# Kernel optimization log

Measured on AMD Instinct MI355X. Metric: run time of the kernel, lower is better.

## Reference

```python
import jax, jax.numpy as jnp
import numpy as np

N = 50000      # nodes
E = 800000     # edges (before self-loops)
F_IN = 128     # num_features
HID = 32       # hidden_channels
HEADS = 4
CLS = 40       # num_classes
NEG_SLOPE = 0.2


def setup_inputs() -> dict:
    key = jax.random.key(0)
    ks = jax.random.split(key, 10)
    s = 0.1
    x = jax.random.normal(ks[0], (N, F_IN), jnp.float32)
    edge_index = jax.random.randint(ks[1], (2, E), 0, N, jnp.int32)
    W1 = jax.random.normal(ks[2], (F_IN, HEADS * HID), jnp.float32) * s
    att_src1 = jax.random.normal(ks[3], (HEADS, HID), jnp.float32) * s
    att_dst1 = jax.random.normal(ks[4], (HEADS, HID), jnp.float32) * s
    b1 = jnp.zeros((HEADS * HID,), jnp.float32)
    W2 = jax.random.normal(ks[5], (HEADS * HID, CLS), jnp.float32) * s
    att_src2 = jax.random.normal(ks[6], (1, CLS), jnp.float32) * s
    att_dst2 = jax.random.normal(ks[7], (1, CLS), jnp.float32) * s
    b2 = jnp.zeros((CLS,), jnp.float32)
    return {"x": x, "edge_index": edge_index,
            "W1": W1, "att_src1": att_src1, "att_dst1": att_dst1, "b1": b1,
            "W2": W2, "att_src2": att_src2, "att_dst2": att_dst2, "b2": b2}


def gat_layer(x, src, dst, W, a_src, a_dst, b, concat):
    """PyG GATConv: per-head linear, edge attention logits a_src.h_j + a_dst.h_i,
    LeakyReLU, segment softmax over incoming edges per dst, weighted scatter-sum."""
    n = x.shape[0]
    H, C = a_src.shape
    h = (x @ W).reshape(n, H, C)                       # [N, H, C]
    al_s = jnp.einsum('nhc,hc->nh', h, a_src)          # [N, H]
    al_d = jnp.einsum('nhc,hc->nh', h, a_dst)          # [N, H]
    e = jax.nn.leaky_relu(al_s[src] + al_d[dst], NEG_SLOPE)  # [E, H]
    e_max = jax.lax.stop_gradient(jax.ops.segment_max(e, dst, num_segments=n))
    e = jnp.exp(e - e_max[dst])
    denom = jax.ops.segment_sum(e, dst, num_segments=n)      # [N, H]
    alpha = e / (denom[dst] + 1e-16)                         # [E, H]
    out = jax.ops.segment_sum(h[src] * alpha[:, :, None], dst, num_segments=n)  # [N, H, C]
    out = out.reshape(n, H * C) if concat else out.mean(axis=1)
    return out + b


def reference(x, edge_index, W1, att_src1, att_dst1, b1, W2, att_src2, att_dst2, b2):
    n = x.shape[0]
    loops = jnp.arange(n, dtype=edge_index.dtype)
    src = jnp.concatenate([edge_index[0], loops])  # PyG adds self-loops by default
    dst = jnp.concatenate([edge_index[1], loops])
    h = gat_layer(x, src, dst, W1, att_src1, att_dst1, b1, concat=True)
    h = jax.nn.relu(h)  # dropout is identity in eval mode
    h = gat_layer(h, src, dst, W2, att_src2, att_dst2, b2, concat=False)
    return jax.nn.log_softmax(h, axis=1)
```

## Files before the change

kernel.cpp:

```cpp
#include <hip/hip_runtime.h>
#include <hip/hip_bf16.h>
#include <cstdint>
#include <cstddef>

#define NN 50000
#define EE 800000
#define ETOT (EE + NN)
#define FIN 128
#define D1 128
#define HEADS 4
#define HID 32
#define CLS 40
#define NEG 0.2f
#define MAXDEG 64
#define NPART 8
#define PSIZE 6250
#define GB 104
#define BGB (NPART * GB)

typedef __attribute__((ext_vector_type(8))) short short8;
typedef __attribute__((ext_vector_type(4))) float float4v;

union U16 { uint4 u; short8 s; };

__device__ __forceinline__ float bf2f(unsigned short u) {
    union { unsigned int i; float f; } v; v.i = ((unsigned int)u) << 16; return v.f;
}
__device__ __forceinline__ unsigned short f2bf(float f) {
    union { unsigned int i; float f; } v; v.f = f;
    unsigned int r = v.i + 0x7fffu + ((v.i >> 16) & 1u);
    return (unsigned short)(r >> 16);
}

__global__ __launch_bounds__(256, 4) void bg_k(const int* __restrict__ eidx,
                                               int* __restrict__ cnt,
                                               unsigned short* __restrict__ ssrcp,
                                               const float* __restrict__ X,
                                               const float* __restrict__ W,
                                               const float* __restrict__ as1,
                                               const float* __restrict__ ad1,
                                               unsigned int* __restrict__ H1b,
                                               float* __restrict__ ALS1,
                                               float* __restrict__ ALD1) {
    __shared__ uint4 Wl[2048];
    __shared__ float sas[128], sad[128];
    int t = threadIdx.x;

    if (blockIdx.x < BGB) {
        int part = blockIdx.x & (NPART - 1);
        int g    = blockIdx.x >> 3;
        int lo = part * PSIZE, hi = lo + PSIZE;
        int stride = GB * 256;
        for (int i = g * 256 + t; i < ETOT; i += stride) {
            int dN = (i < EE) ? eidx[EE + i] : (i - EE);
            if (dN >= lo && dN < hi) {
                int sN = (i < EE) ? eidx[i] : dN;
                int slot = atomicAdd(&cnt[dN], 1);
                if (slot < MAXDEG) ssrcp[dN * MAXDEG + slot] = (unsigned short)sN;
            }
        }
        return;
    }

    int bI = blockIdx.x - BGB;
    if (t < 128) { sas[t] = as1[t]; sad[t] = ad1[t]; }
    for (int g = t; g < 2048; g += 256) {
        int ct = g >> 8, rem = g & 255, kc = rem >> 6, l = rem & 63;
        int c = ct * 16 + (l & 15);
        int k0 = kc * 32 + (l >> 4) * 8;
        U16 u;
#pragma unroll
        for (int j = 0; j < 8; j++) u.s[j] = (short)f2bf(W[(k0 + j) * D1 + c]);
        Wl[g] = u.u;
    }
    __syncthreads();

    int wid = t >> 6, lane = t & 63, quad = lane >> 4, lrow = lane & 15;
    int wrow0 = bI * 128 + wid * 32;

    short8 afr[2][4];
#pragma unroll
    for (int rt = 0; rt < 2; rt++) {
        int r = wrow0 + rt * 16 + lrow;
#pragma unroll
        for (int kc = 0; kc < 4; kc++) {
            short8 a = {0, 0, 0, 0, 0, 0, 0, 0};
            if (r < NN) {
                const float* xp = X + (size_t)r * FIN + kc * 32 + quad * 8;
                float4 x0 = *(const float4*)xp;
                float4 x1 = *(const float4*)(xp + 4);
                a[0] = (short)f2bf(x0.x); a[1] = (short)f2bf(x0.y);
                a[2] = (short)f2bf(x0.z); a[3] = (short)f2bf(x0.w);
                a[4] = (short)f2bf(x1.x); a[5] = (short)f2bf(x1.y);
                a[6] = (short)f2bf(x1.z); a[7] = (short)f2bf(x1.w);
            }
            afr[rt][kc] = a;
        }
    }

    float4v acc[2][4];

    for (int cp = 0; cp < 2; ++cp) {
#pragma unroll
        for (int rt = 0; rt < 2; rt++)
#pragma unroll
            for (int c4 = 0; c4 < 4; c4++) acc[rt][c4] = (float4v)(0.f);

#pragma unroll
        for (int c4 = 0; c4 < 4; c4++) {
#pragma unroll
            for (int kc = 0; kc < 4; kc++) {
                U16 b; b.u = Wl[((cp * 4 + c4) * 4 + kc) * 64 + lane];
                acc[0][c4] = __builtin_amdgcn_mfma_f32_16x16x32_bf16(afr[0][kc], b.s, acc[0][c4], 0, 0, 0);
                acc[1][c4] = __builtin_amdgcn_mfma_f32_16x16x32_bf16(afr[1][kc], b.s, acc[1][c4], 0, 0, 0);
            }
        }

#pragma unroll
        for (int rt = 0; rt < 2; rt++) {
#pragma unroll
            for (int reg = 0; reg < 4; reg++) {
                float ps[2] = {0.f, 0.f};
                float pd[2] = {0.f, 0.f};
#pragma unroll
                for (int c4 = 0; c4 < 4; c4++) {
                    float v = acc[rt][c4][reg];
                    int ct = cp * 4 + c4;
                    ps[c4 >> 1] += v * sas[ct * 16 + lrow];
                    pd[c4 >> 1] += v * sad[ct * 16 + lrow];
                }
#pragma unroll
                for (int o = 1; o < 16; o <<= 1) {
#pragma unroll
                    for (int h = 0; h < 2; h++) {
                        ps[h] += __shfl_xor(ps[h], o);
                        pd[h] += __shfl_xor(pd[h], o);
                    }
                }
                int r = wrow0 + rt * 16 + quad * 4 + reg;
                if (lrow == 0 && r < NN) {
                    *(float2*)&ALS1[(size_t)r * 4 + cp * 2] = make_float2(ps[0], ps[1]);
                    *(float2*)&ALD1[(size_t)r * 4 + cp * 2] = make_float2(pd[0], pd[1]);
                }
            }
        }

#pragma unroll
        for (int rt = 0; rt < 2; rt++)
#pragma unroll
            for (int c4 = 0; c4 < 4; c4++)
#pragma unroll
                for (int reg = 0; reg < 4; reg++) {
                    float v = acc[rt][c4][reg];
                    float o = __shfl_xor(v, 1);
                    int r = wrow0 + rt * 16 + quad * 4 + reg;
                    if (((lane & 1) == 0) && r < NN) {
                        unsigned int u = (unsigned int)f2bf(v) | ((unsigned int)f2bf(o) << 16);
                        H1b[(size_t)r * 64 + (cp * 4 + c4) * 8 + (lrow >> 1)] = u;
                    }
                }
    }
}

__global__ __launch_bounds__(256) void gather1_k(const int* __restrict__ cnt,
                                                 const unsigned short* __restrict__ ssrcp,
                                                 const uint4* __restrict__ H1b4,
                                                 const float4* __restrict__ ALS,
                                                 const float4* __restrict__ ALD,
                                                 const float* __restrict__ b1,
                                                 uint4* __restrict__ OUT1b4) {
    __shared__ float wlds[4][MAXDEG][4];
    __shared__ int sidlds[4][MAXDEG];
    int wid = threadIdx.x >> 6, lane = threadIdx.x & 63;
    int v = blockIdx.x * 4 + wid;
    int deg = min(cnt[v], MAXDEG);
    float4 ad = ALD[v];
    float w0 = 0.f, w1 = 0.f, w2 = 0.f, w3 = 0.f;
    if (lane < deg) {
        int s = (int)ssrcp[v * MAXDEG + lane];
        sidlds[wid][lane] = s;
        float4 as = ALS[s];
        float l0 = as.x + ad.x; l0 = l0 > 0.f ? l0 : NEG * l0;
        float l1 = as.y + ad.y; l1 = l1 > 0.f ? l1 : NEG * l1;
        float l2 = as.z + ad.z; l2 = l2 > 0.f ? l2 : NEG * l2;
        float l3 = as.w + ad.w; l3 = l3 > 0.f ? l3 : NEG * l3;
        w0 = __expf(l0); w1 = __expf(l1); w2 = __expf(l2); w3 = __expf(l3);
        wlds[wid][lane][0] = w0; wlds[wid][lane][1] = w1;
        wlds[wid][lane][2] = w2; wlds[wid][lane][3] = w3;
    }
    float d0 = w0, d1 = w1, d2 = w2, d3 = w3;
#pragma unroll
    for (int o = 1; o < 64; o <<= 1) {
        d0 += __shfl_xor(d0, o); d1 += __shfl_xor(d1, o);
        d2 += __shfl_xor(d2, o); d3 += __shfl_xor(d3, o);
    }
    __syncthreads();
    int g = lane >> 4, l = lane & 15, head = l >> 2;
    float a0=0.f,a1=0.f,a2=0.f,a3=0.f,a4=0.f,a5=0.f,a6=0.f,a7=0.f;
    for (int j = g; j < deg; j += 4) {
        float wj = wlds[wid][j][head];
        int s = sidlds[wid][j];
        uint4 q = H1b4[(size_t)s * 16 + l];
        a0 += wj * bf2f((unsigned short)(q.x & 0xffffu));
        a1 += wj * bf2f((unsigned short)(q.x >> 16));
        a2 += wj * bf2f((unsigned short)(q.y & 0xffffu));
        a3 += wj * bf2f((unsigned short)(q.y >> 16));
        a4 += wj * bf2f((unsigned short)(q.z & 0xffffu));
        a5 += wj * bf2f((unsigned short)(q.z >> 16));
        a6 += wj * bf2f((unsigned short)(q.w & 0xffffu));
        a7 += wj * bf2f((unsigned short)(q.w >> 16));
    }
#pragma unroll
    for (int o = 16; o < 64; o <<= 1) {
        a0 += __shfl_xor(a0, o); a1 += __shfl_xor(a1, o);
        a2 += __shfl_xor(a2, o); a3 += __shfl_xor(a3, o);
        a4 += __shfl_xor(a4, o); a5 += __shfl_xor(a5, o);
        a6 += __shfl_xor(a6, o); a7 += __shfl_xor(a7, o);
    }
    if (lane < 16) {
        float den = (head == 0) ? d0 : (head == 1) ? d1 : (head == 2) ? d2 : d3;
        den += 1e-16f;
        float4 bA = *(const float4*)&b1[8 * l];
        float4 bB = *(const float4*)&b1[8 * l + 4];
        float o0 = fmaxf(a0 / den + bA.x, 0.f);
        float o1 = fmaxf(a1 / den + bA.y, 0.f);
        float o2 = fmaxf(a2 / den + bA.z, 0.f);
        float o3 = fmaxf(a3 / den + bA.w, 0.f);
        float o4 = fmaxf(a4 / den + bB.x, 0.f);
        float o5 = fmaxf(a5 / den + bB.y, 0.f);
        float o6 = fmaxf(a6 / den + bB.z, 0.f);
        float o7 = fmaxf(a7 / den + bB.w, 0.f);
        uint4 u;
        u.x = (unsigned int)f2bf(o0) | ((unsigned int)f2bf(o1) << 16);
        u.y = (unsigned int)f2bf(o2) | ((unsigned int)f2bf(o3) << 16);
        u.z = (unsigned int)f2bf(o4) | ((unsigned int)f2bf(o5) << 16);
        u.w = (unsigned int)f2bf(o6) | ((unsigned int)f2bf(o7) << 16);
        OUT1b4[(size_t)v * 16 + l] = u;
    }
}

__global__ __launch_bounds__(256) void gemm2_k(const unsigned int* __restrict__ OUT1b,
                                               const float* __restrict__ W2,
                                               const float* __restrict__ as2,
                                               const float* __restrict__ ad2,
                                               unsigned int* __restrict__ H2b,
                                               float* __restrict__ ALS2,
                                               float* __restrict__ ALD2) {
    __shared__ uint4 Wl[768];
    __shared__ float sas[48], sad[48];
    int t = threadIdx.x;
    if (t < 48) {
        sas[t] = (t < CLS) ? as2[t] : 0.f;
        sad[t] = (t < CLS) ? ad2[t] : 0.f;
    }
    for (int g = t; g < 768; g += 256) {
        int ct = g >> 8, rem = g & 255, kc = rem >> 6, l = rem & 63;
        int c = ct * 16 + (l & 15);
        int k0 = kc * 32 + (l >> 4) * 8;
        U16 u;
#pragma unroll
        for (int j = 0; j < 8; j++)
            u.s[j] = (c < CLS) ? (short)f2bf(W2[(k0 + j) * CLS + c]) : (short)0;
        Wl[g] = u.u;
    }
    __syncthreads();

    int wid = t >> 6, lane = t & 63, quad = lane >> 4, lrow = lane & 15;
    int wrow0 = blockIdx.x * 128 + wid * 32;

    U16 afr[2][4];
#pragma unroll
    for (int rt = 0; rt < 2; rt++) {
        int r = wrow0 + rt * 16 + lrow;
#pragma unroll
        for (int kc = 0; kc < 4; kc++) {
            if (r < NN)
                afr[rt][kc].u = ((const uint4*)OUT1b)[(size_t)r * 16 + kc * 4 + quad];
            else
                afr[rt][kc].u = make_uint4(0, 0, 0, 0);
        }
    }

    float4v acc[2][3];
#pragma unroll
    for (int rt = 0; rt < 2; rt++)
#pragma unroll
        for (int ct = 0; ct < 3; ct++) acc[rt][ct] = (float4v)(0.f);

#pragma unroll
    for (int ct = 0; ct < 3; ct++) {
#pragma unroll
        for (int kc = 0; kc < 4; kc++) {
            U16 b; b.u = Wl[(ct * 4 + kc) * 64 + lane];
            acc[0][ct] = __builtin_amdgcn_mfma_f32_16x16x32_bf16(afr[0][kc].s, b.s, acc[0][ct], 0, 0, 0);
            acc[1][ct] = __builtin_amdgcn_mfma_f32_16x16x32_bf16(afr[1][kc].s, b.s, acc[1][ct], 0, 0, 0);
        }
    }

#pragma unroll
    for (int rt = 0; rt < 2; rt++) {
#pragma unroll
        for (int reg = 0; reg < 4; reg++) {
            float ps = 0.f, pd = 0.f;
#pragma unroll
            for (int ct = 0; ct < 3; ct++) {
                float v = acc[rt][ct][reg];
                ps += v * sas[ct * 16 + lrow];
                pd += v * sad[ct * 16 + lrow];
            }
#pragma unroll
            for (int o = 1; o < 16; o <<= 1) {
                ps += __shfl_xor(ps, o);
                pd += __shfl_xor(pd, o);
            }
            int r = wrow0 + rt * 16 + quad * 4 + reg;
            if (lrow == 0 && r < NN) {
                ALS2[r] = ps;
                ALD2[r] = pd;
            }
        }
    }

#pragma unroll
    for (int rt = 0; rt < 2; rt++)
#pragma unroll
        for (int ct = 0; ct < 3; ct++)
#pragma unroll
            for (int reg = 0; reg < 4; reg++) {
                float v = acc[rt][ct][reg];
                float o = __shfl_xor(v, 1);
                int r = wrow0 + rt * 16 + quad * 4 + reg;
                int c = ct * 16 + lrow;
                if (((lane & 1) == 0) && c < CLS && r < NN) {
                    unsigned int u = (unsigned int)f2bf(v) | ((unsigned int)f2bf(o) << 16);
                    H2b[(size_t)r * 20 + (c >> 1)] = u;
                }
            }
}

__global__ __launch_bounds__(256) void gather2_k(const int* __restrict__ cnt,
                                                 const unsigned short* __restrict__ ssrcp,
                                                 const unsigned int* __restrict__ H2b,
                                                 const float* __restrict__ ALS,
                                                 const float* __restrict__ ALD,
                                                 const float* __restrict__ b2,
                                                 float* __restrict__ out) {
    int wid = threadIdx.x >> 6, t = threadIdx.x & 63;
    int v = blockIdx.x * 4 + wid;
    int deg = min(cnt[v], MAXDEG);
    __shared__ float w[4][MAXDEG];
    __shared__ int sid[4][MAXDEG];
    __shared__ float part[4][2][CLS];
    float den = 0.f;
    float adv = ALD[v];
    if (t < deg) {
        int s = (int)ssrcp[(size_t)v * MAXDEG + t];
        sid[wid][t] = s;
        float l = ALS[s] + adv; l = l > 0.f ? l : NEG * l;
        float e = __expf(l);
        w[wid][t] = e; den = e;
    }
    __syncthreads();
    int g = t >> 5, c = t & 31;
    if (c < 20) {
        float ax = 0.f, ay = 0.f;
        for (int j = g; j < deg; j += 2) {
            float wj = w[wid][j];
            unsigned int u = H2b[(size_t)sid[wid][j] * 20 + c];
            ax += wj * bf2f((unsigned short)(u & 0xffffu));
            ay += wj * bf2f((unsigned short)(u >> 16));
        }
        part[wid][g][2 * c] = ax;
        part[wid][g][2 * c + 1] = ay;
    }
#pragma unroll
    for (int o = 32; o > 0; o >>= 1) den += __shfl_xor(den, o);
    __syncthreads();
    float z = (t < CLS) ? (part[wid][0][t] + part[wid][1][t]) / (den + 1e-16f) + b2[t] : -1e30f;
    float mx = z;
#pragma unroll
    for (int o = 32; o > 0; o >>= 1) mx = fmaxf(mx, __shfl_xor(mx, o));
    float ex = (t < CLS) ? __expf(z - mx) : 0.f;
    float se = ex;
#pragma unroll
    for (int o = 32; o > 0; o >>= 1) se += __shfl_xor(se, o);
    if (t < CLS) out[(size_t)v * CLS + t] = z - mx - __logf(se);
}

extern "C" void kernel_launch(void* const* d_in, const int* in_sizes, int n_in,
                              void* d_out, int out_size, void* d_ws, size_t ws_size,
                              hipStream_t stream) {
    const float* x   = (const float*)d_in[0];
    const int*   eix = (const int*)d_in[1];
    const float* W1  = (const float*)d_in[2];
    const float* as1 = (const float*)d_in[3];
    const float* ad1 = (const float*)d_in[4];
    const float* b1  = (const float*)d_in[5];
    const float* W2  = (const float*)d_in[6];
    const float* as2 = (const float*)d_in[7];
    const float* ad2 = (const float*)d_in[8];
    const float* b2  = (const float*)d_in[9];
    float* out = (float*)d_out;

    char* p = (char*)d_ws;
    auto carve = [&](size_t bytes) -> void* {
        void* r = (void*)p;
        p += (bytes + 255) & ~(size_t)255;
        return r;
    };
    unsigned int* H1b   = (unsigned int*)carve((size_t)NN * 64 * 4);
    unsigned int* OUT1b = (unsigned int*)carve((size_t)NN * 64 * 4);
    unsigned int* H2b   = (unsigned int*)carve((size_t)NN * 20 * 4);
    float* ALS1 = (float*)carve((size_t)NN * 4 * 4);
    float* ALD1 = (float*)carve((size_t)NN * 4 * 4);
    float* ALS2 = (float*)carve((size_t)NN * 4);
    float* ALD2 = (float*)carve((size_t)NN * 4);
    int* cnt    = (int*)carve((size_t)NN * 4);
    unsigned short* ssrcp = (unsigned short*)carve((size_t)NN * MAXDEG * 2);

    hipMemsetAsync(cnt, 0, (size_t)NN * 4, stream);

    int gemmBlocks = (NN + 127) / 128;
    bg_k<<<BGB + gemmBlocks, 256, 0, stream>>>(eix, cnt, ssrcp, x, W1, as1, ad1,
                                               H1b, ALS1, ALD1);
    gather1_k<<<NN / 4, 256, 0, stream>>>(cnt, ssrcp, (const uint4*)H1b,
                                          (const float4*)ALS1, (const float4*)ALD1,
                                          b1, (uint4*)OUT1b);
    gemm2_k<<<(NN + 127) / 128, 256, 0, stream>>>(OUT1b, W2, as2, ad2, H2b, ALS2, ALD2);
    gather2_k<<<NN / 4, 256, 0, stream>>>(cnt, ssrcp, H2b, ALS2, ALD2, b2, out);
}
```

Before: 226.1 us.

## Vectorize edge bucketing, implicit self-loops, and batch gather loads four-deep

The edge-bucketing phase no longer makes every block scan all edges filtered by a destination partition. Each thread now reads int4 chunks of src/dst and performs four atomics, and self-loops are no longer stored but added implicitly in both gather kernels. The gather loops issue four independent row loads per iteration to increase memory-level parallelism, and gather2 uses three edge groups of 20 lanes instead of two of 32. The risk is more scattered atomic and store traffic without partition locality, plus higher register pressure.

```diff
diff --git a/kernel.cpp b/kernel.cpp
--- a/kernel.cpp
+++ b/kernel.cpp
@@ -5,7 +5,6 @@
 
 #define NN 50000
 #define EE 800000
-#define ETOT (EE + NN)
 #define FIN 128
 #define D1 128
 #define HEADS 4
@@ -13,10 +12,7 @@
 #define CLS 40
 #define NEG 0.2f
 #define MAXDEG 64
-#define NPART 8
-#define PSIZE 6250
-#define GB 104
-#define BGB (NPART * GB)
+#define BGB 632
 
 typedef __attribute__((ext_vector_type(8))) short short8;
 typedef __attribute__((ext_vector_type(4))) float float4v;
@@ -47,17 +43,20 @@
     int t = threadIdx.x;
 
     if (blockIdx.x < BGB) {
-        int part = blockIdx.x & (NPART - 1);
-        int g    = blockIdx.x >> 3;
-        int lo = part * PSIZE, hi = lo + PSIZE;
-        int stride = GB * 256;
-        for (int i = g * 256 + t; i < ETOT; i += stride) {
-            int dN = (i < EE) ? eidx[EE + i] : (i - EE);
-            if (dN >= lo && dN < hi) {
-                int sN = (i < EE) ? eidx[i] : dN;
-                int slot = atomicAdd(&cnt[dN], 1);
-                if (slot < MAXDEG) ssrcp[dN * MAXDEG + slot] = (unsigned short)sN;
-            }
+        const int4* src4 = (const int4*)eidx;
+        const int4* dst4 = (const int4*)(eidx + EE);
+        int stride = BGB * 256;
+        for (int i4 = blockIdx.x * 256 + t; i4 < EE / 4; i4 += stride) {
+            int4 d = dst4[i4];
+            int4 s = src4[i4];
+            int s0 = atomicAdd(&cnt[d.x], 1);
+            int s1 = atomicAdd(&cnt[d.y], 1);
+            int s2 = atomicAdd(&cnt[d.z], 1);
+            int s3 = atomicAdd(&cnt[d.w], 1);
+            if (s0 < MAXDEG - 1) ssrcp[(size_t)d.x * MAXDEG + s0] = (unsigned short)s.x;
+            if (s1 < MAXDEG - 1) ssrcp[(size_t)d.y * MAXDEG + s1] = (unsigned short)s.y;
+            if (s2 < MAXDEG - 1) ssrcp[(size_t)d.z * MAXDEG + s2] = (unsigned short)s.z;
+            if (s3 < MAXDEG - 1) ssrcp[(size_t)d.w * MAXDEG + s3] = (unsigned short)s.w;
         }
         return;
     }
@@ -173,11 +172,12 @@
     __shared__ int sidlds[4][MAXDEG];
     int wid = threadIdx.x >> 6, lane = threadIdx.x & 63;
     int v = blockIdx.x * 4 + wid;
-    int deg = min(cnt[v], MAXDEG);
+    int degE = min(cnt[v], MAXDEG - 1);
+    int degT = degE + 1;
     float4 ad = ALD[v];
     float w0 = 0.f, w1 = 0.f, w2 = 0.f, w3 = 0.f;
-    if (lane < deg) {
-        int s = (int)ssrcp[v * MAXDEG + lane];
+    if (lane < degT) {
+        int s = (lane < degE) ? (int)ssrcp[(size_t)v * MAXDEG + lane] : v;
         sidlds[wid][lane] = s;
         float4 as = ALS[s];
         float l0 = as.x + ad.x; l0 = l0 > 0.f ? l0 : NEG * l0;
@@ -197,18 +197,35 @@
     __syncthreads();
     int g = lane >> 4, l = lane & 15, head = l >> 2;
     float a0=0.f,a1=0.f,a2=0.f,a3=0.f,a4=0.f,a5=0.f,a6=0.f,a7=0.f;
-    for (int j = g; j < deg; j += 4) {
-        float wj = wlds[wid][j][head];
-        int s = sidlds[wid][j];
-        uint4 q = H1b4[(size_t)s * 16 + l];
-        a0 += wj * bf2f((unsigned short)(q.x & 0xffffu));
-        a1 += wj * bf2f((unsigned short)(q.x >> 16));
-        a2 += wj * bf2f((unsigned short)(q.y & 0xffffu));
-        a3 += wj * bf2f((unsigned short)(q.y >> 16));
-        a4 += wj * bf2f((unsigned short)(q.z & 0xffffu));
-        a5 += wj * bf2f((unsigned short)(q.z >> 16));
-        a6 += wj * bf2f((unsigned short)(q.w & 0xffffu));
-        a7 += wj * bf2f((unsigned short)(q.w >> 16));
+    {
+        int j0 = g, j1 = g + 4, j2 = g + 8, j3 = g + 12;
+        uint4 q0 = make_uint4(0,0,0,0), q1 = q0, q2 = q0, q3 = q0;
+        float p0 = 0.f, p1 = 0.f, p2 = 0.f, p3 = 0.f;
+        if (j0 < degT) { p0 = wlds[wid][j0][head]; q0 = H1b4[(size_t)sidlds[wid][j0] * 16 + l]; }
+        if (j1 < degT) { p1 = wlds[wid][j1][head]; q1 = H1b4[(size_t)sidlds[wid][j1] * 16 + l]; }
+        if (j2 < degT) { p2 = wlds[wid][j2][head]; q2 = H1b4[(size_t)sidlds[wid][j2] * 16 + l]; }
+        if (j3 < degT) { p3 = wlds[wid][j3][head]; q3 = H1b4[(size_t)sidlds[wid][j3] * 16 + l]; }
+        for (;;) {
+#define ACC8(Q, P)                                           \
+            a0 += (P) * bf2f((unsigned short)((Q).x & 0xffffu)); \
+            a1 += (P) * bf2f((unsigned short)((Q).x >> 16));     \
+            a2 += (P) * bf2f((unsigned short)((Q).y & 0xffffu)); \
+            a3 += (P) * bf2f((unsigned short)((Q).y >> 16));     \
+            a4 += (P) * bf2f((unsigned short)((Q).z & 0xffffu)); \
+            a5 += (P) * bf2f((unsigned short)((Q).z >> 16));     \
+            a6 += (P) * bf2f((unsigned short)((Q).w & 0xffffu)); \
+            a7 += (P) * bf2f((unsigned short)((Q).w >> 16));
+            ACC8(q0, p0) ACC8(q1, p1) ACC8(q2, p2) ACC8(q3, p3)
+#undef ACC8
+            j0 += 16;
+            if (j0 >= degT) break;
+            j1 += 16; j2 += 16; j3 += 16;
+            p0 = 0.f; p1 = 0.f; p2 = 0.f; p3 = 0.f;
+            { p0 = wlds[wid][j0][head]; q0 = H1b4[(size_t)sidlds[wid][j0] * 16 + l]; }
+            if (j1 < degT) { p1 = wlds[wid][j1][head]; q1 = H1b4[(size_t)sidlds[wid][j1] * 16 + l]; }
+            if (j2 < degT) { p2 = wlds[wid][j2][head]; q2 = H1b4[(size_t)sidlds[wid][j2] * 16 + l]; }
+            if (j3 < degT) { p3 = wlds[wid][j3][head]; q3 = H1b4[(size_t)sidlds[wid][j3] * 16 + l]; }
+        }
     }
 #pragma unroll
     for (int o = 16; o < 64; o <<= 1) {
@@ -347,28 +364,48 @@
                                                  float* __restrict__ out) {
     int wid = threadIdx.x >> 6, t = threadIdx.x & 63;
     int v = blockIdx.x * 4 + wid;
-    int deg = min(cnt[v], MAXDEG);
+    int degE = min(cnt[v], MAXDEG - 1);
+    int degT = degE + 1;
     __shared__ float w[4][MAXDEG];
     __shared__ int sid[4][MAXDEG];
-    __shared__ float part[4][2][CLS];
+    __shared__ float part[4][3][CLS];
     float den = 0.f;
     float adv = ALD[v];
-    if (t < deg) {
-        int s = (int)ssrcp[(size_t)v * MAXDEG + t];
+    if (t < degT) {
+        int s = (t < degE) ? (int)ssrcp[(size_t)v * MAXDEG + t] : v;
         sid[wid][t] = s;
         float l = ALS[s] + adv; l = l > 0.f ? l : NEG * l;
         float e = __expf(l);
         w[wid][t] = e; den = e;
     }
     __syncthreads();
-    int g = t >> 5, c = t & 31;
-    if (c < 20) {
+    int g = t / 20, c = t % 20;
+    if (t < 60) {
         float ax = 0.f, ay = 0.f;
-        for (int j = g; j < deg; j += 2) {
-            float wj = w[wid][j];
-            unsigned int u = H2b[(size_t)sid[wid][j] * 20 + c];
-            ax += wj * bf2f((unsigned short)(u & 0xffffu));
-            ay += wj * bf2f((unsigned short)(u >> 16));
+        int j0 = g, j1 = g + 3, j2 = g + 6, j3 = g + 9;
+        unsigned int u0 = 0u, u1 = 0u, u2 = 0u, u3 = 0u;
+        float p0 = 0.f, p1 = 0.f, p2 = 0.f, p3 = 0.f;
+        if (j0 < degT) { p0 = w[wid][j0]; u0 = H2b[(size_t)sid[wid][j0] * 20 + c]; }
+        if (j1 < degT) { p1 = w[wid][j1]; u1 = H2b[(size_t)sid[wid][j1] * 20 + c]; }
+        if (j2 < degT) { p2 = w[wid][j2]; u2 = H2b[(size_t)sid[wid][j2] * 20 + c]; }
+        if (j3 < degT) { p3 = w[wid][j3]; u3 = H2b[(size_t)sid[wid][j3] * 20 + c]; }
+        for (;;) {
+            ax += p0 * bf2f((unsigned short)(u0 & 0xffffu));
+            ay += p0 * bf2f((unsigned short)(u0 >> 16));
+            ax += p1 * bf2f((unsigned short)(u1 & 0xffffu));
+            ay += p1 * bf2f((unsigned short)(u1 >> 16));
+            ax += p2 * bf2f((unsigned short)(u2 & 0xffffu));
+            ay += p2 * bf2f((unsigned short)(u2 >> 16));
+            ax += p3 * bf2f((unsigned short)(u3 & 0xffffu));
+            ay += p3 * bf2f((unsigned short)(u3 >> 16));
+            j0 += 12;
+            if (j0 >= degT) break;
+            j1 += 12; j2 += 12; j3 += 12;
+            p0 = 0.f; p1 = 0.f; p2 = 0.f; p3 = 0.f;
+            { p0 = w[wid][j0]; u0 = H2b[(size_t)sid[wid][j0] * 20 + c]; }
+            if (j1 < degT) { p1 = w[wid][j1]; u1 = H2b[(size_t)sid[wid][j1] * 20 + c]; }
+            if (j2 < degT) { p2 = w[wid][j2]; u2 = H2b[(size_t)sid[wid][j2] * 20 + c]; }
+            if (j3 < degT) { p3 = w[wid][j3]; u3 = H2b[(size_t)sid[wid][j3] * 20 + c]; }
         }
         part[wid][g][2 * c] = ax;
         part[wid][g][2 * c + 1] = ay;
@@ -376,7 +413,8 @@
 #pragma unroll
     for (int o = 32; o > 0; o >>= 1) den += __shfl_xor(den, o);
     __syncthreads();
-    float z = (t < CLS) ? (part[wid][0][t] + part[wid][1][t]) / (den + 1e-16f) + b2[t] : -1e30f;
+    float z = (t < CLS) ? (part[wid][0][t] + part[wid][1][t] + part[wid][2][t]) / (den + 1e-16f) + b2[t]
+                        : -1e30f;
     float mx = z;
 #pragma unroll
     for (int o = 32; o > 0; o >>= 1) mx = fmaxf(mx, __shfl_xor(mx, o));
```

Measured after the change: 226.7 us. About the same (+0.2%).
